# Kernel optimization log

Hardware: AMD Instinct MI355X
Metric: run time of the kernel (lower is better)

## Reference

```python
import jax, jax.numpy as jnp
import numpy as np
import math

NUM_HEADS = 16
LOGIT_SCALE_MAX = math.log(1.0 / 0.01)  # log(100)
EPS = 1e-12


def _l2norm(x):
    # F.normalize(x, dim=-1): x / max(||x||_2, eps)
    n = jnp.sqrt(jnp.sum(x * x, axis=-1, keepdims=True))
    return x / jnp.maximum(n, EPS)


def setup_inputs() -> dict:
    key = jax.random.key(0)
    ks = jax.random.split(key, 6)
    N, B, C = 1024, 4, 1024
    scale = (C // NUM_HEADS) ** -0.5
    return {
        "query": jax.random.normal(ks[0], (N, B, C), jnp.float32),
        "key": jax.random.normal(ks[1], (N, B, C), jnp.float32),
        "value": jax.random.normal(ks[2], (N, B, C), jnp.float32),
        "in_proj_w": jax.random.normal(ks[3], (3 * C, C), jnp.float32) * scale,
        "in_proj_b": jnp.zeros((3 * C,), jnp.float32),
        "logit_scale": jnp.log(10.0) * jnp.ones((NUM_HEADS, 1, 1), jnp.float32),
        "out_w": jax.random.normal(ks[4], (C, C), jnp.float32) * scale,
        "out_b": jnp.zeros((C,), jnp.float32),
    }


def reference(query, key, value, in_proj_w, in_proj_b, logit_scale, out_w, out_b):
    N, B, C = query.shape
    H = NUM_HEADS
    hd = C // H
    # packed in-projection, split into q/k/v pieces
    w_q, w_k, w_v = jnp.split(in_proj_w, 3, axis=0)
    b_q, b_k, b_v = jnp.split(in_proj_b, 3, axis=0)
    q = query @ w_q.T + b_q          # (N, B, C)
    k = key @ w_k.T + b_k
    v = value @ w_v.T + b_v
    # (N, B, C) -> (B*H, N, hd)
    q = q.reshape(N, B * H, hd).swapaxes(0, 1)
    k = k.reshape(N, B * H, hd).swapaxes(0, 1)
    v = v.reshape(N, B * H, hd).swapaxes(0, 1)
    # cosine-similarity scores with learnable per-head logit scale
    attn = jnp.einsum('bqd,bkd->bqk', _l2norm(q), _l2norm(k))  # (B*H, N, N)
    ls = jnp.exp(jnp.minimum(logit_scale, LOGIT_SCALE_MAX))     # (H,1,1)
    attn = (attn.reshape(B, H, N, N) * ls).reshape(B * H, N, N)
    attn = jax.nn.softmax(attn, axis=-1)
    x = jnp.einsum('bqk,bkd->bqd', attn, v)                     # (B*H, N, hd)
    x = x.swapaxes(0, 1).reshape(N, B, C)
    return x @ out_w.T + out_b
```

## Files before the change

kernel.cpp:

```cpp
#include <hip/hip_runtime.h>


typedef _Float16 f16x8 __attribute__((ext_vector_type(8)));
typedef float    f32x4 __attribute__((ext_vector_type(4)));

#define LOG2E 1.4426950408889634f
#define LOGMAX 4.6051702f

__device__ __forceinline__ unsigned short f2h(float x) {
    union { _Float16 h; unsigned short u; } cv;
    cv.h = (_Float16)x;
    return cv.u;
}

__global__ __launch_bounds__(256) void cvt_all(
    const float* __restrict__ q, const float* __restrict__ k,
    const float* __restrict__ v, const float* __restrict__ w,
    const float* __restrict__ ow,
    unsigned short* __restrict__ qbf, unsigned short* __restrict__ kbf,
    unsigned short* __restrict__ vbf, unsigned short* __restrict__ wbf,
    unsigned short* __restrict__ owbf)
{
    int b = blockIdx.x;
    const float* src; unsigned short* dst; int idx;
    if      (b < 4096)  { src = q;  dst = qbf;  idx = b; }
    else if (b < 8192)  { src = k;  dst = kbf;  idx = b - 4096; }
    else if (b < 12288) { src = v;  dst = vbf;  idx = b - 8192; }
    else if (b < 15360) { src = w;  dst = wbf;  idx = b - 12288; }
    else                { src = ow; dst = owbf; idx = b - 15360; }
    int i = idx * 256 + threadIdx.x;
    float4 val = ((const float4*)src)[i];
    ushort4 o;
    o.x = f2h(val.x); o.y = f2h(val.y); o.z = f2h(val.z); o.w = f2h(val.w);
    ((ushort4*)dst)[i] = o;
}

__global__ __launch_bounds__(256) void proj_gemm(
    const unsigned short* __restrict__ qbf, const unsigned short* __restrict__ kbf,
    const unsigned short* __restrict__ vbf, const unsigned short* __restrict__ wbf,
    const float* __restrict__ bias, const float* __restrict__ lsc,
    unsigned short* __restrict__ qn, unsigned short* __restrict__ kn,
    unsigned short* __restrict__ vT)
{
    __shared__ __align__(16) unsigned short Asm[128][72];
    __shared__ __align__(16) unsigned short Bsm[128][72];
    int tid = threadIdx.x;
    int lane = tid & 63, wave = tid >> 6;
    int lr = lane & 15, lq = lane >> 4;
    int wr = wave >> 1, wc = wave & 1;
    int z = blockIdx.z;
    const unsigned short* A = (z == 0) ? qbf : (z == 1) ? kbf : vbf;
    const unsigned short* W = wbf + (size_t)z * 1024 * 1024;
    int m0 = blockIdx.y * 128, n0 = blockIdx.x * 128;

    f32x4 acc[4][4];
    for (int i = 0; i < 4; i++) for (int j = 0; j < 4; j++) acc[i][j] = (f32x4){0.f, 0.f, 0.f, 0.f};

    for (int ki = 0; ki < 16; ++ki) {
        for (int c = tid; c < 1024; c += 256) {
            int row = c >> 3, off = (c & 7) << 3;
            *(uint4*)&Asm[row][off] = *(const uint4*)(A + (size_t)(m0 + row) * 1024 + ki * 64 + off);
            *(uint4*)&Bsm[row][off] = *(const uint4*)(W + (size_t)(n0 + row) * 1024 + ki * 64 + off);
        }
        __syncthreads();
        for (int kc = 0; kc < 2; ++kc) {
            f16x8 af[4], bfr[4];
            for (int mi = 0; mi < 4; ++mi) af[mi]  = *(const f16x8*)&Asm[wr * 64 + mi * 16 + lr][kc * 32 + lq * 8];
            for (int ni = 0; ni < 4; ++ni) bfr[ni] = *(const f16x8*)&Bsm[wc * 64 + ni * 16 + lr][kc * 32 + lq * 8];
            for (int mi = 0; mi < 4; ++mi)
                for (int ni = 0; ni < 4; ++ni)
                    acc[mi][ni] = __builtin_amdgcn_mfma_f32_16x16x32_f16(af[mi], bfr[ni], acc[mi][ni], 0, 0, 0);
        }
        __syncthreads();
    }

    int h = (n0 >> 6) + wc;
    float bv[4];
    for (int ni = 0; ni < 4; ++ni) bv[ni] = bias[z * 1024 + n0 + wc * 64 + ni * 16 + lr];
    for (int mi = 0; mi < 4; ++mi)
        for (int ni = 0; ni < 4; ++ni)
            for (int r = 0; r < 4; ++r) acc[mi][ni][r] += bv[ni];

    float lsfac = __expf(fminf(lsc[h], LOGMAX)) * LOG2E;

    for (int mi = 0; mi < 4; ++mi)
        for (int r = 0; r < 4; ++r) {
            int row = m0 + wr * 64 + mi * 16 + lq * 4 + r;
            int n = row >> 2, b = row & 3;
            int bh = b * 16 + h;
            if (z < 2) {
                float ss = 0.f;
                for (int ni = 0; ni < 4; ++ni) ss += acc[mi][ni][r] * acc[mi][ni][r];
                for (int off = 1; off < 16; off <<= 1) ss += __shfl_xor(ss, off);
                float scale = 1.0f / fmaxf(sqrtf(ss), 1e-12f);
                if (z == 0) scale *= lsfac;
                unsigned short* dst = (z == 0) ? qn : kn;
                for (int ni = 0; ni < 4; ++ni)
                    dst[(size_t)bh * 65536 + (size_t)n * 64 + ni * 16 + lr] = f2h(acc[mi][ni][r] * scale);
            } else {
                for (int ni = 0; ni < 4; ++ni)
                    vT[(size_t)bh * 65536 + (size_t)(ni * 16 + lr) * 1024 + n] = f2h(acc[mi][ni][r]);
            }
        }
}

__global__ __launch_bounds__(256) void flash_kernel(
    const unsigned short* __restrict__ qn, const unsigned short* __restrict__ kn,
    const unsigned short* __restrict__ vT, const float* __restrict__ lsc,
    unsigned short* __restrict__ xb)
{
    __shared__ __align__(16) unsigned short K_lds[64][72];
    __shared__ __align__(16) unsigned short V_lds[64][72];
    __shared__ __align__(16) unsigned short P_lds[4][16][72];
    int tid = threadIdx.x;
    int lane = tid & 63, wave = tid >> 6;
    int lr = lane & 15, lq = lane >> 4;
    int qt = blockIdx.x, bh = blockIdx.y;
    int q0 = qt * 64 + wave * 16;

    float off = __expf(fminf(lsc[bh & 15], LOGMAX)) * LOG2E - 12.0f;

    f16x8 qf[2];
    for (int kc = 0; kc < 2; ++kc)
        qf[kc] = *(const f16x8*)(qn + (size_t)bh * 65536 + (size_t)(q0 + lr) * 64 + kc * 32 + lq * 8);

    f32x4 o[4];
    for (int i = 0; i < 4; i++) o[i] = (f32x4){0.f, 0.f, 0.f, 0.f};
    float lsum = 0.f;

    for (int kt = 0; kt < 16; ++kt) {
        for (int c = tid; c < 512; c += 256) {
            int row = c >> 3, off4 = (c & 7) << 3;
            *(uint4*)&K_lds[row][off4] = *(const uint4*)(kn + (size_t)bh * 65536 + (size_t)(kt * 64 + row) * 64 + off4);
            *(uint4*)&V_lds[row][off4] = *(const uint4*)(vT + (size_t)bh * 65536 + (size_t)row * 1024 + kt * 64 + off4);
        }
        __syncthreads();

        f32x4 s[4];
        for (int ct = 0; ct < 4; ++ct) {
            f32x4 a = (f32x4){0.f, 0.f, 0.f, 0.f};
            for (int kc = 0; kc < 2; ++kc) {
                f16x8 kf = *(const f16x8*)&K_lds[ct * 16 + lr][kc * 32 + lq * 8];
                a = __builtin_amdgcn_mfma_f32_16x16x32_f16(kf, qf[kc], a, 0, 0, 0);
            }
            s[ct] = a;
        }

        for (int ct = 0; ct < 4; ++ct) {
            float p0 = exp2f(s[ct][0] - off), p1 = exp2f(s[ct][1] - off);
            float p2 = exp2f(s[ct][2] - off), p3 = exp2f(s[ct][3] - off);
            lsum += (p0 + p1) + (p2 + p3);
            ushort4 pw;
            pw.x = f2h(p0); pw.y = f2h(p1); pw.z = f2h(p2); pw.w = f2h(p3);
            *(ushort4*)&P_lds[wave][lr][ct * 16 + lq * 4] = pw;
        }

        f16x8 pf[2];
        for (int kc = 0; kc < 2; ++kc)
            pf[kc] = *(const f16x8*)&P_lds[wave][lr][kc * 32 + lq * 8];
        for (int nt = 0; nt < 4; ++nt)
            for (int kc = 0; kc < 2; ++kc) {
                f16x8 vf = *(const f16x8*)&V_lds[nt * 16 + lr][kc * 32 + lq * 8];
                o[nt] = __builtin_amdgcn_mfma_f32_16x16x32_f16(vf, pf[kc], o[nt], 0, 0, 0);
            }
        __syncthreads();
    }

    lsum += __shfl_xor(lsum, 16);
    lsum += __shfl_xor(lsum, 32);
    float inv = 1.0f / lsum;

    for (int nt = 0; nt < 4; ++nt) {
        ushort4 w;
        w.x = f2h(o[nt][0] * inv); w.y = f2h(o[nt][1] * inv);
        w.z = f2h(o[nt][2] * inv); w.w = f2h(o[nt][3] * inv);
        *(ushort4*)(xb + (size_t)bh * 65536 + (size_t)(q0 + lr) * 64 + nt * 16 + lq * 4) = w;
    }
}

__global__ __launch_bounds__(256) void out_gemm(
    const unsigned short* __restrict__ xb, const unsigned short* __restrict__ owbf,
    const float* __restrict__ bias, float* __restrict__ outp)
{
    __shared__ __align__(16) unsigned short Asm[128][72];
    __shared__ __align__(16) unsigned short Bsm[128][72];
    int tid = threadIdx.x;
    int lane = tid & 63, wave = tid >> 6;
    int lr = lane & 15, lq = lane >> 4;
    int wr = wave >> 1, wc = wave & 1;
    int m0 = blockIdx.y * 128, n0 = blockIdx.x * 128;

    f32x4 acc[4][4];
    for (int i = 0; i < 4; i++) for (int j = 0; j < 4; j++) acc[i][j] = (f32x4){0.f, 0.f, 0.f, 0.f};

    for (int ki = 0; ki < 16; ++ki) {
        for (int c = tid; c < 1024; c += 256) {
            int row = c >> 3, off = (c & 7) << 3;
            int grow = m0 + row;
            int b = grow & 3, n = grow >> 2;
            *(uint4*)&Asm[row][off] = *(const uint4*)(xb + (size_t)(b * 16 + ki) * 65536 + (size_t)n * 64 + off);
            *(uint4*)&Bsm[row][off] = *(const uint4*)(owbf + (size_t)(n0 + row) * 1024 + ki * 64 + off);
        }
        __syncthreads();
        for (int kc = 0; kc < 2; ++kc) {
            f16x8 af[4], bfr[4];
            for (int mi = 0; mi < 4; ++mi) af[mi]  = *(const f16x8*)&Asm[wr * 64 + mi * 16 + lr][kc * 32 + lq * 8];
            for (int ni = 0; ni < 4; ++ni) bfr[ni] = *(const f16x8*)&Bsm[wc * 64 + ni * 16 + lr][kc * 32 + lq * 8];
            for (int mi = 0; mi < 4; ++mi)
                for (int ni = 0; ni < 4; ++ni)
                    acc[mi][ni] = __builtin_amdgcn_mfma_f32_16x16x32_f16(af[mi], bfr[ni], acc[mi][ni], 0, 0, 0);
        }
        __syncthreads();
    }
    for (int mi = 0; mi < 4; ++mi)
        for (int ni = 0; ni < 4; ++ni)
            for (int r = 0; r < 4; ++r) {
                int row = m0 + wr * 64 + mi * 16 + lq * 4 + r;
                int col = n0 + wc * 64 + ni * 16 + lr;
                outp[(size_t)row * 1024 + col] = acc[mi][ni][r] + bias[col];
            }
}

extern "C" void kernel_launch(void* const* d_in, const int* in_sizes, int n_in,
                              void* d_out, int out_size, void* d_ws, size_t ws_size,
                              hipStream_t stream) {
    const float* query = (const float*)d_in[0];
    const float* key   = (const float*)d_in[1];
    const float* value = (const float*)d_in[2];
    const float* ipw   = (const float*)d_in[3];
    const float* ipb   = (const float*)d_in[4];
    const float* lsc   = (const float*)d_in[5];
    const float* ow    = (const float*)d_in[6];
    const float* ob    = (const float*)d_in[7];
    float* outp = (float*)d_out;

    char* ws = (char*)d_ws;
    unsigned short* qbf  = (unsigned short*)(ws);
    unsigned short* kbf  = (unsigned short*)(ws + 8388608);
    unsigned short* vbf  = (unsigned short*)(ws + 16777216);
    unsigned short* wbf  = (unsigned short*)(ws + 25165824);
    unsigned short* owbf = (unsigned short*)(ws + 31457280);
    unsigned short* qn   = (unsigned short*)(ws + 33554432);
    unsigned short* kn   = (unsigned short*)(ws + 41943040);
    unsigned short* vT   = (unsigned short*)(ws + 50331648);
    unsigned short* xbuf = (unsigned short*)(ws + 58720256);

    cvt_all<<<16384, 256, 0, stream>>>(query, key, value, ipw, ow,
                                       qbf, kbf, vbf, wbf, owbf);
    proj_gemm<<<dim3(8, 32, 3), 256, 0, stream>>>(qbf, kbf, vbf, wbf, ipb, lsc,
                                                  qn, kn, vT);
    flash_kernel<<<dim3(16, 64), 256, 0, stream>>>(qn, kn, vT, lsc, xbuf);
    out_gemm<<<dim3(8, 32), 256, 0, stream>>>(xbuf, owbf, ob, outp);
}
```

Baseline: 240.9 us.

## Use direct global-to-LDS loads with XOR swizzle and re-tile output GEMM

Replaces register-staged global-to-shared copies in the projection GEMM, flash kernel and output GEMM with global_load_lds direct transfers into an unpadded, XOR-swizzled LDS layout, and reads fragments through the same swizzle to avoid bank conflicts. The flash kernel now writes its output in (N*B, C) row-major order so the output GEMM can load contiguous rows. The output GEMM moves to 128x64 tiles with a 16x32 grid to get more blocks. This is meant to cut VGPR pressure and load instructions and to improve occupancy, at the cost of relying on correct swizzle and per-wave load mapping.

```diff
diff --git a/kernel.cpp b/kernel.cpp
--- a/kernel.cpp
+++ b/kernel.cpp
@@ -6,6 +6,10 @@
 
 #define LOG2E 1.4426950408889634f
 #define LOGMAX 4.6051702f
+
+#define GLOAD16(g, l) \
+    __builtin_amdgcn_global_load_lds((__attribute__((address_space(1))) void*)(g), \
+                                     (__attribute__((address_space(3))) void*)(l), 16, 0, 0)
 
 __device__ __forceinline__ unsigned short f2h(float x) {
     union { _Float16 h; unsigned short u; } cv;
@@ -42,8 +46,8 @@
     unsigned short* __restrict__ qn, unsigned short* __restrict__ kn,
     unsigned short* __restrict__ vT)
 {
-    __shared__ __align__(16) unsigned short Asm[128][72];
-    __shared__ __align__(16) unsigned short Bsm[128][72];
+    __shared__ __align__(16) unsigned short AsmF[128 * 64];
+    __shared__ __align__(16) unsigned short BsmF[128 * 64];
     int tid = threadIdx.x;
     int lane = tid & 63, wave = tid >> 6;
     int lr = lane & 15, lq = lane >> 4;
@@ -53,20 +57,31 @@
     const unsigned short* W = wbf + (size_t)z * 1024 * 1024;
     int m0 = blockIdx.y * 128, n0 = blockIdx.x * 128;
 
+    int rl = lane >> 3;
+    int cg = ((lane & 7) ^ rl) << 3;
+    const unsigned short* gA = A + (size_t)(m0 + wave * 32 + rl) * 1024 + cg;
+    const unsigned short* gB = W + (size_t)(n0 + wave * 32 + rl) * 1024 + cg;
+    unsigned short* lA = &AsmF[wave * 32 * 64];
+    unsigned short* lB = &BsmF[wave * 32 * 64];
+
+    int swz = lr & 7;
+    int c0 = (lq ^ swz) << 3;
+    int c1 = ((lq ^ 4) ^ swz) << 3;
+
     f32x4 acc[4][4];
     for (int i = 0; i < 4; i++) for (int j = 0; j < 4; j++) acc[i][j] = (f32x4){0.f, 0.f, 0.f, 0.f};
 
     for (int ki = 0; ki < 16; ++ki) {
-        for (int c = tid; c < 1024; c += 256) {
-            int row = c >> 3, off = (c & 7) << 3;
-            *(uint4*)&Asm[row][off] = *(const uint4*)(A + (size_t)(m0 + row) * 1024 + ki * 64 + off);
-            *(uint4*)&Bsm[row][off] = *(const uint4*)(W + (size_t)(n0 + row) * 1024 + ki * 64 + off);
+        for (int j = 0; j < 4; ++j) {
+            GLOAD16(gA + ki * 64 + j * 8192, lA + j * 512);
+            GLOAD16(gB + ki * 64 + j * 8192, lB + j * 512);
         }
         __syncthreads();
         for (int kc = 0; kc < 2; ++kc) {
+            int co = kc ? c1 : c0;
             f16x8 af[4], bfr[4];
-            for (int mi = 0; mi < 4; ++mi) af[mi]  = *(const f16x8*)&Asm[wr * 64 + mi * 16 + lr][kc * 32 + lq * 8];
-            for (int ni = 0; ni < 4; ++ni) bfr[ni] = *(const f16x8*)&Bsm[wc * 64 + ni * 16 + lr][kc * 32 + lq * 8];
+            for (int mi = 0; mi < 4; ++mi) af[mi]  = *(const f16x8*)&AsmF[(wr * 64 + mi * 16 + lr) * 64 + co];
+            for (int ni = 0; ni < 4; ++ni) bfr[ni] = *(const f16x8*)&BsmF[(wc * 64 + ni * 16 + lr) * 64 + co];
             for (int mi = 0; mi < 4; ++mi)
                 for (int ni = 0; ni < 4; ++ni)
                     acc[mi][ni] = __builtin_amdgcn_mfma_f32_16x16x32_f16(af[mi], bfr[ni], acc[mi][ni], 0, 0, 0);
@@ -109,8 +124,8 @@
     const unsigned short* __restrict__ vT, const float* __restrict__ lsc,
     unsigned short* __restrict__ xb)
 {
-    __shared__ __align__(16) unsigned short K_lds[64][72];
-    __shared__ __align__(16) unsigned short V_lds[64][72];
+    __shared__ __align__(16) unsigned short K_flat[64 * 64];
+    __shared__ __align__(16) unsigned short V_flat[64 * 64];
     __shared__ __align__(16) unsigned short P_lds[4][16][72];
     int tid = threadIdx.x;
     int lane = tid & 63, wave = tid >> 6;
@@ -124,15 +139,24 @@
     for (int kc = 0; kc < 2; ++kc)
         qf[kc] = *(const f16x8*)(qn + (size_t)bh * 65536 + (size_t)(q0 + lr) * 64 + kc * 32 + lq * 8);
 
+    int rl = lane >> 3;
+    int cg = ((lane & 7) ^ rl) << 3;
+    const unsigned short* gK = kn + (size_t)bh * 65536 + (size_t)(wave * 16 + rl) * 64 + cg;
+    const unsigned short* gV = vT + (size_t)bh * 65536 + (size_t)(wave * 16 + rl) * 1024 + cg;
+    unsigned short* lK = &K_flat[wave * 16 * 64];
+    unsigned short* lV = &V_flat[wave * 16 * 64];
+    int swz = lr & 7;
+    int c0 = (lq ^ swz) << 3;
+    int c1 = ((lq ^ 4) ^ swz) << 3;
+
     f32x4 o[4];
     for (int i = 0; i < 4; i++) o[i] = (f32x4){0.f, 0.f, 0.f, 0.f};
     float lsum = 0.f;
 
     for (int kt = 0; kt < 16; ++kt) {
-        for (int c = tid; c < 512; c += 256) {
-            int row = c >> 3, off4 = (c & 7) << 3;
-            *(uint4*)&K_lds[row][off4] = *(const uint4*)(kn + (size_t)bh * 65536 + (size_t)(kt * 64 + row) * 64 + off4);
-            *(uint4*)&V_lds[row][off4] = *(const uint4*)(vT + (size_t)bh * 65536 + (size_t)row * 1024 + kt * 64 + off4);
+        for (int j = 0; j < 2; ++j) {
+            GLOAD16(gK + kt * 4096 + j * 512,  lK + j * 512);
+            GLOAD16(gV + kt * 64  + j * 8192,  lV + j * 512);
         }
         __syncthreads();
 
@@ -140,7 +164,7 @@
         for (int ct = 0; ct < 4; ++ct) {
             f32x4 a = (f32x4){0.f, 0.f, 0.f, 0.f};
             for (int kc = 0; kc < 2; ++kc) {
-                f16x8 kf = *(const f16x8*)&K_lds[ct * 16 + lr][kc * 32 + lq * 8];
+                f16x8 kf = *(const f16x8*)&K_flat[(ct * 16 + lr) * 64 + (kc ? c1 : c0)];
                 a = __builtin_amdgcn_mfma_f32_16x16x32_f16(kf, qf[kc], a, 0, 0, 0);
             }
             s[ct] = a;
@@ -160,7 +184,7 @@
             pf[kc] = *(const f16x8*)&P_lds[wave][lr][kc * 32 + lq * 8];
         for (int nt = 0; nt < 4; ++nt)
             for (int kc = 0; kc < 2; ++kc) {
-                f16x8 vf = *(const f16x8*)&V_lds[nt * 16 + lr][kc * 32 + lq * 8];
+                f16x8 vf = *(const f16x8*)&V_flat[(nt * 16 + lr) * 64 + (kc ? c1 : c0)];
                 o[nt] = __builtin_amdgcn_mfma_f32_16x16x32_f16(vf, pf[kc], o[nt], 0, 0, 0);
             }
         __syncthreads();
@@ -170,11 +194,13 @@
     lsum += __shfl_xor(lsum, 32);
     float inv = 1.0f / lsum;
 
+    int b = bh >> 4, h = bh & 15;
     for (int nt = 0; nt < 4; ++nt) {
         ushort4 w;
         w.x = f2h(o[nt][0] * inv); w.y = f2h(o[nt][1] * inv);
         w.z = f2h(o[nt][2] * inv); w.w = f2h(o[nt][3] * inv);
-        *(ushort4*)(xb + (size_t)bh * 65536 + (size_t)(q0 + lr) * 64 + nt * 16 + lq * 4) = w;
+        size_t m = (size_t)(q0 + lr) * 4 + b;
+        *(ushort4*)(xb + m * 1024 + h * 64 + nt * 16 + lq * 4) = w;
     }
 }
 
@@ -182,41 +208,48 @@
     const unsigned short* __restrict__ xb, const unsigned short* __restrict__ owbf,
     const float* __restrict__ bias, float* __restrict__ outp)
 {
-    __shared__ __align__(16) unsigned short Asm[128][72];
-    __shared__ __align__(16) unsigned short Bsm[128][72];
+    __shared__ __align__(16) unsigned short AsmF[128 * 64];
+    __shared__ __align__(16) unsigned short BsmF[64 * 64];
     int tid = threadIdx.x;
     int lane = tid & 63, wave = tid >> 6;
     int lr = lane & 15, lq = lane >> 4;
-    int wr = wave >> 1, wc = wave & 1;
-    int m0 = blockIdx.y * 128, n0 = blockIdx.x * 128;
-
-    f32x4 acc[4][4];
-    for (int i = 0; i < 4; i++) for (int j = 0; j < 4; j++) acc[i][j] = (f32x4){0.f, 0.f, 0.f, 0.f};
+    int m0 = blockIdx.y * 128, n0 = blockIdx.x * 64;
+
+    int rl = lane >> 3;
+    int cg = ((lane & 7) ^ rl) << 3;
+    const unsigned short* gA = xb   + (size_t)(m0 + wave * 32 + rl) * 1024 + cg;
+    const unsigned short* gB = owbf + (size_t)(n0 + wave * 16 + rl) * 1024 + cg;
+    unsigned short* lA = &AsmF[wave * 32 * 64];
+    unsigned short* lB = &BsmF[wave * 16 * 64];
+    int swz = lr & 7;
+    int c0 = (lq ^ swz) << 3;
+    int c1 = ((lq ^ 4) ^ swz) << 3;
+
+    f32x4 acc[2][4];
+    for (int i = 0; i < 2; i++) for (int j = 0; j < 4; j++) acc[i][j] = (f32x4){0.f, 0.f, 0.f, 0.f};
 
     for (int ki = 0; ki < 16; ++ki) {
-        for (int c = tid; c < 1024; c += 256) {
-            int row = c >> 3, off = (c & 7) << 3;
-            int grow = m0 + row;
-            int b = grow & 3, n = grow >> 2;
-            *(uint4*)&Asm[row][off] = *(const uint4*)(xb + (size_t)(b * 16 + ki) * 65536 + (size_t)n * 64 + off);
-            *(uint4*)&Bsm[row][off] = *(const uint4*)(owbf + (size_t)(n0 + row) * 1024 + ki * 64 + off);
-        }
+        for (int j = 0; j < 4; ++j)
+            GLOAD16(gA + ki * 64 + j * 8192, lA + j * 512);
+        for (int j = 0; j < 2; ++j)
+            GLOAD16(gB + ki * 64 + j * 8192, lB + j * 512);
         __syncthreads();
         for (int kc = 0; kc < 2; ++kc) {
-            f16x8 af[4], bfr[4];
-            for (int mi = 0; mi < 4; ++mi) af[mi]  = *(const f16x8*)&Asm[wr * 64 + mi * 16 + lr][kc * 32 + lq * 8];
-            for (int ni = 0; ni < 4; ++ni) bfr[ni] = *(const f16x8*)&Bsm[wc * 64 + ni * 16 + lr][kc * 32 + lq * 8];
-            for (int mi = 0; mi < 4; ++mi)
+            int co = kc ? c1 : c0;
+            f16x8 af[2], bfr[4];
+            for (int mi = 0; mi < 2; ++mi) af[mi]  = *(const f16x8*)&AsmF[(wave * 32 + mi * 16 + lr) * 64 + co];
+            for (int ni = 0; ni < 4; ++ni) bfr[ni] = *(const f16x8*)&BsmF[(ni * 16 + lr) * 64 + co];
+            for (int mi = 0; mi < 2; ++mi)
                 for (int ni = 0; ni < 4; ++ni)
                     acc[mi][ni] = __builtin_amdgcn_mfma_f32_16x16x32_f16(af[mi], bfr[ni], acc[mi][ni], 0, 0, 0);
         }
         __syncthreads();
     }
-    for (int mi = 0; mi < 4; ++mi)
+    for (int mi = 0; mi < 2; ++mi)
         for (int ni = 0; ni < 4; ++ni)
             for (int r = 0; r < 4; ++r) {
-                int row = m0 + wr * 64 + mi * 16 + lq * 4 + r;
-                int col = n0 + wc * 64 + ni * 16 + lr;
+                int row = m0 + wave * 32 + mi * 16 + lq * 4 + r;
+                int col = n0 + ni * 16 + lr;
                 outp[(size_t)row * 1024 + col] = acc[mi][ni][r] + bias[col];
             }
 }
@@ -250,5 +283,5 @@
     proj_gemm<<<dim3(8, 32, 3), 256, 0, stream>>>(qbf, kbf, vbf, wbf, ipb, lsc,
                                                   qn, kn, vT);
     flash_kernel<<<dim3(16, 64), 256, 0, stream>>>(qn, kn, vT, lsc, xbuf);
-    out_gemm<<<dim3(8, 32), 256, 0, stream>>>(xbuf, owbf, ob, outp);
-}
+    out_gemm<<<dim3(16, 32), 256, 0, stream>>>(xbuf, owbf, ob, outp);
+}
```

Result: faster. 218.4 us (-9.3%).
